# Kernel tuning notes

Hardware: AMD Instinct MI355X
Metric: run time of the kernel (lower is better)

The kernel has to match this reference:

```python
import jax, jax.numpy as jnp
import numpy as np

C = 256

def setup_inputs() -> dict:
    key = jax.random.key(0)
    ks = jax.random.split(key, 9)
    B, H, W = 32, 32, 32
    s = C ** -0.5  # init scale for weights
    inputs = jax.random.normal(ks[0], (B, H, W, C), jnp.float32)
    Wq = jax.random.normal(ks[1], (C, C), jnp.float32) * s
    Wk = jax.random.normal(ks[2], (C, C), jnp.float32) * s
    Wv = jax.random.normal(ks[3], (C, C), jnp.float32) * s
    Wo = jax.random.normal(ks[4], (C, C), jnp.float32) * s
    bq = jnp.zeros((C,), jnp.float32)
    bk = jnp.zeros((C,), jnp.float32)
    bv = jnp.zeros((C,), jnp.float32)
    bo = jnp.zeros((C,), jnp.float32)
    return {"inputs": inputs, "Wq": Wq, "bq": bq, "Wk": Wk, "bk": bk,
            "Wv": Wv, "bv": bv, "Wo": Wo, "bo": bo}

def reference(inputs, Wq, bq, Wk, bk, Wv, bv, Wo, bo):
    B, H, W, c = inputs.shape
    scale = jnp.float32(c) ** -0.5
    x = inputs.reshape(B, H * W, c)           # 1x1 conv == per-pixel matmul
    q = x @ Wq + bq                           # [B, HW, C]
    k = x @ Wk + bk
    v = x @ Wv + bv
    scores = jnp.einsum('bnc,bmc->bnm', q, k) * scale  # [B, HW, HW]
    attn = jax.nn.softmax(scores, axis=-1)
    attended = jnp.einsum('bnm,bmc->bnc', attn, v)     # [B, HW, C]
    out = attended @ Wo + bo
    return out.reshape(B, H, W, c)
```

## Files before the change

kernel.cpp:

```cpp
#include <hip/hip_runtime.h>
#include <hip/hip_bf16.h>

typedef __bf16 bf16;
typedef __bf16 bf16x4 __attribute__((ext_vector_type(4)));
typedef __bf16 bf16x8 __attribute__((ext_vector_type(8)));
typedef float f32x4 __attribute__((ext_vector_type(4)));

#define SM_C 0.09016994374947424f

__global__ __launch_bounds__(256) void transpose_w(
    const float* __restrict__ Wq, const float* __restrict__ Wk,
    const float* __restrict__ Wv, const float* __restrict__ Wo,
    bf16* __restrict__ Wt)
{
    int idx = blockIdx.x * 256 + threadIdx.x;
    int m = idx >> 16, r = idx & 65535;
    int n = r >> 8, k = r & 255;
    const float* W = (m == 0) ? Wq : (m == 1) ? Wk : (m == 2) ? Wv : Wo;
    Wt[(size_t)m * 65536 + n * 256 + k] = (bf16)W[k * 256 + n];
}

__global__ __launch_bounds__(256, 3) void qkv_gemm(
    const float* __restrict__ X, const bf16* __restrict__ Wt,
    const float* __restrict__ bq, const float* __restrict__ bk,
    const float* __restrict__ bv,
    bf16* __restrict__ Qo, bf16* __restrict__ Ko, bf16* __restrict__ Vto)
{
    __shared__ bf16 Xs[128 * 72];
    __shared__ bf16 Ws_[128 * 72];

    const int t    = threadIdx.x;
    const int lane = t & 63, wv = t >> 6;
    const int quad = lane >> 4, l16 = lane & 15;
    const int bm   = blockIdx.x;
    const int bn   = blockIdx.y;
    const int proj = bn >> 1;

    const bf16* W = Wt + (size_t)proj * 65536 + (size_t)(bn & 1) * 32768;
    const float* bias = (proj == 0) ? bq : (proj == 1) ? bk : bv;

    const int m0 = t >> 3;
    const int c0 = (t & 7) * 8;

    const f32x4 zero = {0.0f, 0.0f, 0.0f, 0.0f};
    f32x4 acc[2][8];
#pragma unroll
    for (int i = 0; i < 2; ++i)
#pragma unroll
        for (int j = 0; j < 8; ++j) acc[i][j] = zero;

    f32x4 xa[4], xb[4]; bf16x8 wp[4];
#pragma unroll
    for (int p = 0; p < 4; ++p) {
        const float* px = X + (size_t)(bm * 128 + m0 + p * 32) * 256 + c0;
        xa[p] = *(const f32x4*)px; xb[p] = *(const f32x4*)(px + 4);
        wp[p] = *(const bf16x8*)(W + (size_t)(m0 + p * 32) * 256 + c0);
    }

    for (int kt = 0; kt < 4; ++kt) {
#pragma unroll
        for (int p = 0; p < 4; ++p) {
            bf16x8 r;
#pragma unroll
            for (int j = 0; j < 4; ++j) { r[j] = (bf16)xa[p][j]; r[j + 4] = (bf16)xb[p][j]; }
            *(bf16x8*)(Xs + (m0 + p * 32) * 72 + c0) = r;
            *(bf16x8*)(Ws_ + (m0 + p * 32) * 72 + c0) = wp[p];
        }
        __syncthreads();

        if (kt < 3) {
#pragma unroll
            for (int p = 0; p < 4; ++p) {
                const float* px = X + (size_t)(bm * 128 + m0 + p * 32) * 256 + (kt + 1) * 64 + c0;
                xa[p] = *(const f32x4*)px; xb[p] = *(const f32x4*)(px + 4);
                wp[p] = *(const bf16x8*)(W + (size_t)(m0 + p * 32) * 256 + (kt + 1) * 64 + c0);
            }
        }

#pragma unroll
        for (int ks = 0; ks < 2; ++ks) {
            bf16x8 a[2], bb[8];
#pragma unroll
            for (int mt = 0; mt < 2; ++mt)
                a[mt] = *(const bf16x8*)(Xs + (wv * 32 + mt * 16 + l16) * 72 + ks * 32 + quad * 8);
#pragma unroll
            for (int nt = 0; nt < 8; ++nt)
                bb[nt] = *(const bf16x8*)(Ws_ + (nt * 16 + l16) * 72 + ks * 32 + quad * 8);
#pragma unroll
            for (int mt = 0; mt < 2; ++mt)
#pragma unroll
                for (int nt = 0; nt < 8; ++nt)
                    acc[mt][nt] = __builtin_amdgcn_mfma_f32_16x16x32_bf16(
                        a[mt], bb[nt], acc[mt][nt], 0, 0, 0);
        }
        __syncthreads();
    }

#pragma unroll
    for (int nt = 0; nt < 8; ++nt) {
        int col = (bn & 1) * 128 + nt * 16 + l16;
        float bvv = bias[col];
#pragma unroll
        for (int mt = 0; mt < 2; ++mt) {
            int grow0 = bm * 128 + wv * 32 + mt * 16 + quad * 4;
            if (proj == 2) {
                bf16x4 pk;
#pragma unroll
                for (int r = 0; r < 4; ++r) pk[r] = (bf16)(acc[mt][nt][r] + bvv);
                int b = grow0 >> 10, m = grow0 & 1023;
                *(bf16x4*)(Vto + (size_t)b * 262144 + (size_t)col * 1024 + m) = pk;
            } else {
                bf16* dst = (proj == 0) ? Qo : Ko;
#pragma unroll
                for (int r = 0; r < 4; ++r)
                    dst[(size_t)(grow0 + r) * 256 + col] = (bf16)(acc[mt][nt][r] + bvv);
            }
        }
    }
}

__global__ __launch_bounds__(512, 2) void flash_attn(
    const bf16* __restrict__ Qr, const bf16* __restrict__ K,
    const bf16* __restrict__ Vt, const bf16* __restrict__ Wo,
    const float* __restrict__ bo, float* __restrict__ out)
{
    __shared__ __align__(16) char smem[142336];
    bf16* const Ksp0 = (bf16*)(smem);
    bf16* const Ksp1 = (bf16*)(smem + 16896);
    bf16* const Vsp0 = (bf16*)(smem + 33792);
    bf16* const Vsp1 = (bf16*)(smem + 54272);
    bf16* const Os   = (bf16*)(smem);
    bf16* const Wos  = (bf16*)(smem + 74752);

    const int t    = threadIdx.x;
    const int lane = t & 63, wv = t >> 6;
    const int quad = lane >> 4, l16 = lane & 15;
    const int b  = blockIdx.x;
    const int qt = blockIdx.y;

    char* const Pb = smem + 74752 + wv * 1024;

    bf16x8 qf[8];
    const size_t qrow = (size_t)b * 1024 + qt * 128 + wv * 16 + l16;
#pragma unroll
    for (int ks = 0; ks < 8; ++ks)
        qf[ks] = *(const bf16x8*)(Qr + qrow * 256 + ks * 32 + quad * 8);

    const f32x4 zero = {0.0f, 0.0f, 0.0f, 0.0f};
    f32x4 o[16];
#pragma unroll
    for (int n = 0; n < 16; ++n) o[n] = zero;
    float lst[4] = {0.f, 0.f, 0.f, 0.f};

    const int kv0 = t >> 4, kc0 = (t & 15) * 8;
    const int vc0 = t >> 1, vm0 = (t & 1) * 8;

    bf16x8 kp[2], vp[2];
#pragma unroll
    for (int p = 0; p < 2; ++p) {
        kp[p] = *(const bf16x8*)(K + (size_t)(b * 1024 + kv0) * 256 + kc0 + p * 128);
        vp[p] = *(const bf16x8*)(Vt + (size_t)b * 262144 + (size_t)vc0 * 1024 + vm0 + p * 16);
    }
#pragma unroll
    for (int p = 0; p < 2; ++p) {
        *(bf16x8*)(Ksp0 + kv0 * 264 + kc0 + p * 128) = kp[p];
        *(bf16x8*)(Vsp0 + vc0 * 40 + vm0 + p * 16) = vp[p];
    }
#pragma unroll
    for (int p = 0; p < 2; ++p) {
        kp[p] = *(const bf16x8*)(K + (size_t)(b * 1024 + 32 + kv0) * 256 + kc0 + p * 128);
        vp[p] = *(const bf16x8*)(Vt + (size_t)b * 262144 + (size_t)vc0 * 1024 + 32 + vm0 + p * 16);
    }

    for (int j = 0; j < 32; ++j) {
        const bf16* Kb = (j & 1) ? Ksp1 : Ksp0;
        const bf16* Vb = (j & 1) ? Vsp1 : Vsp0;
        __syncthreads();

        f32x4 s[2];
        s[0] = zero; s[1] = zero;
#pragma unroll
        for (int ks = 0; ks < 8; ++ks) {
#pragma unroll
            for (int n = 0; n < 2; ++n) {
                bf16x8 bfr = *(const bf16x8*)(Kb + (n * 16 + l16) * 264 + ks * 32 + quad * 8);
                s[n] = __builtin_amdgcn_mfma_f32_16x16x32_bf16(qf[ks], bfr, s[n], 0, 0, 0);
            }
        }

        if (j < 31) {
            bf16* Kn = (j & 1) ? Ksp0 : Ksp1;
            bf16* Vn = (j & 1) ? Vsp0 : Vsp1;
#pragma unroll
            for (int p = 0; p < 2; ++p) {
                *(bf16x8*)(Kn + kv0 * 264 + kc0 + p * 128) = kp[p];
                *(bf16x8*)(Vn + vc0 * 40 + vm0 + p * 16) = vp[p];
            }
            if (j < 30) {
#pragma unroll
                for (int p = 0; p < 2; ++p) {
                    kp[p] = *(const bf16x8*)(K + (size_t)(b * 1024 + (j + 2) * 32 + kv0) * 256 + kc0 + p * 128);
                    vp[p] = *(const bf16x8*)(Vt + (size_t)b * 262144 + (size_t)vc0 * 1024 + (j + 2) * 32 + vm0 + p * 16);
                }
            }
        }

#pragma unroll
        for (int n = 0; n < 2; ++n) {
#pragma unroll
            for (int r = 0; r < 4; ++r) {
                float pv = __builtin_amdgcn_exp2f(s[n][r] * SM_C);
                lst[r] += pv;
                int row = quad * 4 + r;
                *(bf16*)(Pb + ((row * 64 + n * 32 + l16 * 2) ^ ((row & 7) << 4))) = (bf16)pv;
            }
        }

        bf16x8 af = *(const bf16x8*)(Pb + ((l16 * 64 + quad * 16) ^ ((l16 & 7) << 4)));
#pragma unroll
        for (int n = 0; n < 16; ++n) {
            bf16x8 bfr = *(const bf16x8*)(Vb + (n * 16 + l16) * 40 + quad * 8);
            o[n] = __builtin_amdgcn_mfma_f32_16x16x32_bf16(af, bfr, o[n], 0, 0, 0);
        }
    }

    __syncthreads();

    float inv[4];
#pragma unroll
    for (int r = 0; r < 4; ++r) {
        float l = lst[r];
#pragma unroll
        for (int off = 1; off < 16; off <<= 1)
            l += __shfl_xor(l, off, 64);
        inv[r] = 1.0f / l;
    }
#pragma unroll
    for (int n = 0; n < 16; ++n)
#pragma unroll
        for (int r = 0; r < 4; ++r)
            Os[(wv * 16 + quad * 4 + r) * 264 + n * 16 + l16] = (bf16)(o[n][r] * inv[r]);

    const int rh = (wv & 1) * 64;
    const int nq = wv >> 1;
    const size_t orow0 = (size_t)b * 1024 + qt * 128 + rh;

#pragma unroll
    for (int h = 0; h < 2; ++h) {
        if (h) __syncthreads();
#pragma unroll
        for (int i = 0; i < 8; ++i) {
            int c = t + i * 512;
            int row = c >> 5, c8 = (c & 31) * 8;
            *(bf16x8*)(Wos + row * 264 + c8) =
                *(const bf16x8*)(Wo + (size_t)(h * 128 + row) * 256 + c8);
        }
        __syncthreads();

        f32x4 acc[4][2];
#pragma unroll
        for (int mt = 0; mt < 4; ++mt) { acc[mt][0] = zero; acc[mt][1] = zero; }

#pragma unroll
        for (int ks = 0; ks < 8; ++ks) {
            bf16x8 a[4], bb[2];
#pragma unroll
            for (int mt = 0; mt < 4; ++mt)
                a[mt] = *(const bf16x8*)(Os + (rh + mt * 16 + l16) * 264 + ks * 32 + quad * 8);
#pragma unroll
            for (int nt = 0; nt < 2; ++nt)
                bb[nt] = *(const bf16x8*)(Wos + (nq * 32 + nt * 16 + l16) * 264 + ks * 32 + quad * 8);
#pragma unroll
            for (int mt = 0; mt < 4; ++mt)
#pragma unroll
                for (int nt = 0; nt < 2; ++nt)
                    acc[mt][nt] = __builtin_amdgcn_mfma_f32_16x16x32_bf16(
                        a[mt], bb[nt], acc[mt][nt], 0, 0, 0);
        }

#pragma unroll
        for (int nt = 0; nt < 2; ++nt) {
            int col = h * 128 + nq * 32 + nt * 16 + l16;
            float bvv = bo[col];
#pragma unroll
            for (int mt = 0; mt < 4; ++mt) {
#pragma unroll
                for (int r = 0; r < 4; ++r) {
                    size_t row = orow0 + mt * 16 + quad * 4 + r;
                    out[row * 256 + col] = acc[mt][nt][r] + bvv;
                }
            }
        }
    }
}

extern "C" void kernel_launch(void* const* d_in, const int* in_sizes, int n_in,
                              void* d_out, int out_size, void* d_ws, size_t ws_size,
                              hipStream_t stream)
{
    (void)in_sizes; (void)n_in; (void)out_size; (void)ws_size;
    const float* X  = (const float*)d_in[0];
    const float* Wq = (const float*)d_in[1];
    const float* bq = (const float*)d_in[2];
    const float* Wk = (const float*)d_in[3];
    const float* bk = (const float*)d_in[4];
    const float* Wv = (const float*)d_in[5];
    const float* bv = (const float*)d_in[6];
    const float* Wo = (const float*)d_in[7];
    const float* bo = (const float*)d_in[8];
    float* out = (float*)d_out;

    const size_t NTOK = (size_t)32768 * 256;

    bf16* Wt  = (bf16*)d_ws;
    bf16* Qw  = (bf16*)d_ws + 262144;
    bf16* Kw  = Qw + NTOK;
    bf16* Vtw = Kw + NTOK;

    transpose_w<<<1024, 256, 0, stream>>>(Wq, Wk, Wv, Wo, Wt);
    qkv_gemm   <<<dim3(256, 6), 256, 0, stream>>>(X, Wt, bq, bk, bv, Qw, Kw, Vtw);
    flash_attn <<<dim3(32, 8),  512, 0, stream>>>(Qw, Kw, Vtw, Wt + 3 * 65536, bo, out);
}
```

Before: 181.8 us.

## Split KV sequence across two wave groups with direct-to-LDS K loads

The attention kernel now splits its 8 waves into two groups that each handle alternating KV tiles, with every wave processing 32 query rows instead of 16. K tiles are loaded with global_load_lds into a swizzled LDS layout, while V stays register-staged. The partial O accumulators and row sums are merged through shared memory before normalization. The weight transpose is also rewritten as a tiled, coalesced shared-memory transpose. This gives more reuse of each K/V fragment across MFMAs, at the cost of more registers, a larger LDS footprint and an extra reduction phase.

```diff
diff --git a/kernel.cpp b/kernel.cpp
--- a/kernel.cpp
+++ b/kernel.cpp
@@ -2,22 +2,39 @@
 #include <hip/hip_bf16.h>
 
 typedef __bf16 bf16;
+typedef __bf16 bf16x2 __attribute__((ext_vector_type(2)));
 typedef __bf16 bf16x4 __attribute__((ext_vector_type(4)));
 typedef __bf16 bf16x8 __attribute__((ext_vector_type(8)));
 typedef float f32x4 __attribute__((ext_vector_type(4)));
 
 #define SM_C 0.09016994374947424f
+
+typedef __attribute__((address_space(1))) const void as1_void;
+typedef __attribute__((address_space(3))) void as3_void;
 
 __global__ __launch_bounds__(256) void transpose_w(
     const float* __restrict__ Wq, const float* __restrict__ Wk,
     const float* __restrict__ Wv, const float* __restrict__ Wo,
     bf16* __restrict__ Wt)
 {
-    int idx = blockIdx.x * 256 + threadIdx.x;
-    int m = idx >> 16, r = idx & 65535;
-    int n = r >> 8, k = r & 255;
+    __shared__ float T[32][33];
+    const int bid = blockIdx.x;
+    const int m = bid >> 6, tile = bid & 63;
+    const int tn0 = (tile >> 3) * 32, tk0 = (tile & 7) * 32;
     const float* W = (m == 0) ? Wq : (m == 1) ? Wk : (m == 2) ? Wv : Wo;
-    Wt[(size_t)m * 65536 + n * 256 + k] = (bf16)W[k * 256 + n];
+
+    const int t = threadIdx.x;
+    const int r = t >> 3, c4 = (t & 7) * 4;
+
+    f32x4 v = *(const f32x4*)(W + (size_t)(tk0 + r) * 256 + tn0 + c4);
+#pragma unroll
+    for (int j = 0; j < 4; ++j) T[r][c4 + j] = v[j];
+    __syncthreads();
+
+    bf16x4 ov;
+#pragma unroll
+    for (int j = 0; j < 4; ++j) ov[j] = (bf16)T[c4 + j][r];
+    *(bf16x4*)(Wt + (size_t)m * 65536 + (size_t)(tn0 + r) * 256 + tk0 + c4) = ov;
 }
 
 __global__ __launch_bounds__(256, 3) void qkv_gemm(
@@ -124,123 +141,190 @@
     const bf16* __restrict__ Vt, const bf16* __restrict__ Wo,
     const float* __restrict__ bo, float* __restrict__ out)
 {
-    __shared__ __align__(16) char smem[142336];
-    bf16* const Ksp0 = (bf16*)(smem);
-    bf16* const Ksp1 = (bf16*)(smem + 16896);
-    bf16* const Vsp0 = (bf16*)(smem + 33792);
-    bf16* const Vsp1 = (bf16*)(smem + 54272);
-    bf16* const Os   = (bf16*)(smem);
-    bf16* const Wos  = (bf16*)(smem + 74752);
+    __shared__ __align__(16) char smem[155648];
 
     const int t    = threadIdx.x;
     const int lane = t & 63, wv = t >> 6;
     const int quad = lane >> 4, l16 = lane & 15;
+    const int g    = wv >> 2, wl = wv & 3;
+    const int gt   = t & 255;
     const int b  = blockIdx.x;
     const int qt = blockIdx.y;
 
-    char* const Pb = smem + 74752 + wv * 1024;
-
-    bf16x8 qf[8];
-    const size_t qrow = (size_t)b * 1024 + qt * 128 + wv * 16 + l16;
-#pragma unroll
-    for (int ks = 0; ks < 8; ++ks)
-        qf[ks] = *(const bf16x8*)(Qr + qrow * 256 + ks * 32 + quad * 8);
+    char* const KsB = smem + g * 73728;
+    char* const VsB = smem + g * 73728 + 32768;
+    char* const Pb  = smem + 147456 + wv * 1024;
+    const int psw = (l16 & 7) << 4;
+
+    bf16x8 qf[2][8];
+#pragma unroll
+    for (int mt = 0; mt < 2; ++mt) {
+        const bf16* qp = Qr + ((size_t)b * 1024 + qt * 128 + wl * 32 + mt * 16 + l16) * 256 + quad * 8;
+#pragma unroll
+        for (int ks = 0; ks < 8; ++ks)
+            qf[mt][ks] = *(const bf16x8*)(qp + ks * 32);
+    }
 
     const f32x4 zero = {0.0f, 0.0f, 0.0f, 0.0f};
-    f32x4 o[16];
-#pragma unroll
-    for (int n = 0; n < 16; ++n) o[n] = zero;
-    float lst[4] = {0.f, 0.f, 0.f, 0.f};
-
-    const int kv0 = t >> 4, kc0 = (t & 15) * 8;
-    const int vc0 = t >> 1, vm0 = (t & 1) * 8;
-
-    bf16x8 kp[2], vp[2];
-#pragma unroll
-    for (int p = 0; p < 2; ++p) {
-        kp[p] = *(const bf16x8*)(K + (size_t)(b * 1024 + kv0) * 256 + kc0 + p * 128);
-        vp[p] = *(const bf16x8*)(Vt + (size_t)b * 262144 + (size_t)vc0 * 1024 + vm0 + p * 16);
-    }
-#pragma unroll
-    for (int p = 0; p < 2; ++p) {
-        *(bf16x8*)(Ksp0 + kv0 * 264 + kc0 + p * 128) = kp[p];
-        *(bf16x8*)(Vsp0 + vc0 * 40 + vm0 + p * 16) = vp[p];
-    }
-#pragma unroll
-    for (int p = 0; p < 2; ++p) {
-        kp[p] = *(const bf16x8*)(K + (size_t)(b * 1024 + 32 + kv0) * 256 + kc0 + p * 128);
-        vp[p] = *(const bf16x8*)(Vt + (size_t)b * 262144 + (size_t)vc0 * 1024 + 32 + vm0 + p * 16);
-    }
-
-    for (int j = 0; j < 32; ++j) {
-        const bf16* Kb = (j & 1) ? Ksp1 : Ksp0;
-        const bf16* Vb = (j & 1) ? Vsp1 : Vsp0;
+    f32x4 o[2][16];
+#pragma unroll
+    for (int mt = 0; mt < 2; ++mt)
+#pragma unroll
+        for (int n = 0; n < 16; ++n) o[mt][n] = zero;
+    float lst[2] = {0.f, 0.f};
+
+    const int vc  = gt >> 1;
+    const int vk8 = (gt & 1) * 8;
+    bf16x8 vp[4];
+
+    auto gloadK = [&](int T, int buf) {
+#pragma unroll
+        for (int p = 0; p < 4; ++p) {
+            int chunk = wl * 4 + p;
+            int row   = chunk * 2 + (lane >> 5);
+            int w16   = (lane & 31) ^ (row & 7);
+            const bf16* gsrc = K + ((size_t)b * 1024 + T * 32 + row) * 256 + w16 * 8;
+            __builtin_amdgcn_global_load_lds((as1_void*)gsrc,
+                (as3_void*)(KsB + buf * 16384 + chunk * 1024), 16, 0, 0);
+        }
+    };
+    auto vload = [&](int T) {
+#pragma unroll
+        for (int p = 0; p < 4; ++p) {
+            int c = vc + 128 * (p >> 1), k8 = vk8 + (p & 1) * 16;
+            vp[p] = *(const bf16x8*)(Vt + (size_t)b * 262144 + (size_t)c * 1024 + T * 32 + k8);
+        }
+    };
+    auto vcommit = [&](int buf) {
+#pragma unroll
+        for (int p = 0; p < 4; ++p) {
+            int c = vc + 128 * (p >> 1), k8 = vk8 + (p & 1) * 16;
+            *(bf16x8*)(VsB + buf * 20480 + c * 80 + k8 * 2) = vp[p];
+        }
+    };
+
+    gloadK(g, 0);
+    vload(g); vcommit(0); vload(g + 2);
+
+    for (int i = 0; i < 16; ++i) {
+        const int buf = i & 1;
         __syncthreads();
 
-        f32x4 s[2];
-        s[0] = zero; s[1] = zero;
+        if (i < 15) {
+            gloadK(g + 2 * (i + 1), buf ^ 1);
+            vcommit(buf ^ 1);
+            if (i < 14) vload(g + 2 * (i + 2));
+        }
+
+        f32x4 s[2][2];
+        s[0][0] = zero; s[0][1] = zero; s[1][0] = zero; s[1][1] = zero;
+        const char* Kbuf = KsB + buf * 16384;
 #pragma unroll
         for (int ks = 0; ks < 8; ++ks) {
 #pragma unroll
             for (int n = 0; n < 2; ++n) {
-                bf16x8 bfr = *(const bf16x8*)(Kb + (n * 16 + l16) * 264 + ks * 32 + quad * 8);
-                s[n] = __builtin_amdgcn_mfma_f32_16x16x32_bf16(qf[ks], bfr, s[n], 0, 0, 0);
-            }
-        }
-
-        if (j < 31) {
-            bf16* Kn = (j & 1) ? Ksp0 : Ksp1;
-            bf16* Vn = (j & 1) ? Vsp0 : Vsp1;
-#pragma unroll
-            for (int p = 0; p < 2; ++p) {
-                *(bf16x8*)(Kn + kv0 * 264 + kc0 + p * 128) = kp[p];
-                *(bf16x8*)(Vn + vc0 * 40 + vm0 + p * 16) = vp[p];
-            }
-            if (j < 30) {
-#pragma unroll
-                for (int p = 0; p < 2; ++p) {
-                    kp[p] = *(const bf16x8*)(K + (size_t)(b * 1024 + (j + 2) * 32 + kv0) * 256 + kc0 + p * 128);
-                    vp[p] = *(const bf16x8*)(Vt + (size_t)b * 262144 + (size_t)vc0 * 1024 + (j + 2) * 32 + vm0 + p * 16);
+                bf16x8 kb = *(const bf16x8*)(Kbuf + (n * 16 + l16) * 512 + ((ks * 64 + quad * 16) ^ psw));
+                s[0][n] = __builtin_amdgcn_mfma_f32_16x16x32_bf16(kb, qf[0][ks], s[0][n], 0, 0, 0);
+                s[1][n] = __builtin_amdgcn_mfma_f32_16x16x32_bf16(kb, qf[1][ks], s[1][n], 0, 0, 0);
+            }
+        }
+
+        bf16x8 af[2];
+#pragma unroll
+        for (int mt = 0; mt < 2; ++mt) {
+#pragma unroll
+            for (int n = 0; n < 2; ++n) {
+#pragma unroll
+                for (int h = 0; h < 2; ++h) {
+                    float p0 = __builtin_amdgcn_exp2f(s[mt][n][2 * h] * SM_C);
+                    float p1 = __builtin_amdgcn_exp2f(s[mt][n][2 * h + 1] * SM_C);
+                    lst[mt] += p0 + p1;
+                    bf16x2 pk; pk[0] = (bf16)p0; pk[1] = (bf16)p1;
+                    *(bf16x2*)(Pb + ((l16 * 64 + n * 32 + quad * 8 + h * 4) ^ psw)) = pk;
                 }
             }
-        }
-
-#pragma unroll
-        for (int n = 0; n < 2; ++n) {
-#pragma unroll
-            for (int r = 0; r < 4; ++r) {
-                float pv = __builtin_amdgcn_exp2f(s[n][r] * SM_C);
-                lst[r] += pv;
-                int row = quad * 4 + r;
-                *(bf16*)(Pb + ((row * 64 + n * 32 + l16 * 2) ^ ((row & 7) << 4))) = (bf16)pv;
-            }
-        }
-
-        bf16x8 af = *(const bf16x8*)(Pb + ((l16 * 64 + quad * 16) ^ ((l16 & 7) << 4)));
+            af[mt] = *(const bf16x8*)(Pb + ((l16 * 64 + quad * 16) ^ psw));
+        }
+
+        const char* Vbuf = VsB + buf * 20480;
 #pragma unroll
         for (int n = 0; n < 16; ++n) {
-            bf16x8 bfr = *(const bf16x8*)(Vb + (n * 16 + l16) * 40 + quad * 8);
-            o[n] = __builtin_amdgcn_mfma_f32_16x16x32_bf16(af, bfr, o[n], 0, 0, 0);
-        }
-    }
-
-    __syncthreads();
-
-    float inv[4];
-#pragma unroll
-    for (int r = 0; r < 4; ++r) {
-        float l = lst[r];
-#pragma unroll
-        for (int off = 1; off < 16; off <<= 1)
-            l += __shfl_xor(l, off, 64);
-        inv[r] = 1.0f / l;
-    }
-#pragma unroll
-    for (int n = 0; n < 16; ++n)
-#pragma unroll
-        for (int r = 0; r < 4; ++r)
-            Os[(wv * 16 + quad * 4 + r) * 264 + n * 16 + l16] = (bf16)(o[n][r] * inv[r]);
-
+            bf16x8 vb = *(const bf16x8*)(Vbuf + (n * 16 + l16) * 80 + quad * 16);
+            o[0][n] = __builtin_amdgcn_mfma_f32_16x16x32_bf16(af[0], vb, o[0][n], 0, 0, 0);
+            o[1][n] = __builtin_amdgcn_mfma_f32_16x16x32_bf16(af[1], vb, o[1][n], 0, 0, 0);
+        }
+    }
+
+    __syncthreads();
+
+#pragma unroll
+    for (int mt = 0; mt < 2; ++mt) {
+        lst[mt] += __shfl_xor(lst[mt], 16, 64);
+        lst[mt] += __shfl_xor(lst[mt], 32, 64);
+    }
+
+    float* const scr  = (float*)(smem + 67584);
+    float* const lstS = (float*)(smem + 135168);
+    bf16*  const Os   = (bf16*)smem;
+
+    if (g == 1) {
+        if (quad == 0) {
+            lstS[wl * 32 + l16]      = lst[0];
+            lstS[wl * 32 + 16 + l16] = lst[1];
+        }
+#pragma unroll
+        for (int mt = 0; mt < 2; ++mt)
+#pragma unroll
+            for (int n = 0; n < 8; ++n)
+                *(f32x4*)(scr + (size_t)(n * 16 + l16) * 132 + wl * 32 + mt * 16 + quad * 4) = o[mt][n];
+    }
+    __syncthreads();
+    if (g == 0) {
+        lst[0] += lstS[wl * 32 + l16];
+        lst[1] += lstS[wl * 32 + 16 + l16];
+#pragma unroll
+        for (int mt = 0; mt < 2; ++mt)
+#pragma unroll
+            for (int n = 0; n < 8; ++n) {
+                f32x4 m = *(const f32x4*)(scr + (size_t)(n * 16 + l16) * 132 + wl * 32 + mt * 16 + quad * 4);
+                o[mt][n] += m;
+            }
+    }
+    __syncthreads();
+    if (g == 1) {
+#pragma unroll
+        for (int mt = 0; mt < 2; ++mt)
+#pragma unroll
+            for (int n = 8; n < 16; ++n)
+                *(f32x4*)(scr + (size_t)((n - 8) * 16 + l16) * 132 + wl * 32 + mt * 16 + quad * 4) = o[mt][n];
+    }
+    __syncthreads();
+    if (g == 0) {
+#pragma unroll
+        for (int mt = 0; mt < 2; ++mt)
+#pragma unroll
+            for (int n = 8; n < 16; ++n) {
+                f32x4 m = *(const f32x4*)(scr + (size_t)((n - 8) * 16 + l16) * 132 + wl * 32 + mt * 16 + quad * 4);
+                o[mt][n] += m;
+            }
+        float inv[2][4];
+#pragma unroll
+        for (int mt = 0; mt < 2; ++mt)
+#pragma unroll
+            for (int r = 0; r < 4; ++r)
+                inv[mt][r] = 1.0f / __shfl(lst[mt], quad * 4 + r, 64);
+#pragma unroll
+        for (int mt = 0; mt < 2; ++mt)
+#pragma unroll
+            for (int n = 0; n < 16; ++n)
+#pragma unroll
+                for (int r = 0; r < 4; ++r)
+                    Os[(size_t)(wl * 32 + mt * 16 + quad * 4 + r) * 264 + n * 16 + l16] =
+                        (bf16)(o[mt][n][r] * inv[mt][r]);
+    }
+    __syncthreads();
+
+    bf16* const Wos = (bf16*)(smem + 67584);
     const int rh = (wv & 1) * 64;
     const int nq = wv >> 1;
     const size_t orow0 = (size_t)b * 1024 + qt * 128 + rh;
@@ -266,7 +350,7 @@
             bf16x8 a[4], bb[2];
 #pragma unroll
             for (int mt = 0; mt < 4; ++mt)
-                a[mt] = *(const bf16x8*)(Os + (rh + mt * 16 + l16) * 264 + ks * 32 + quad * 8);
+                a[mt] = *(const bf16x8*)(Os + (size_t)(rh + mt * 16 + l16) * 264 + ks * 32 + quad * 8);
 #pragma unroll
             for (int nt = 0; nt < 2; ++nt)
                 bb[nt] = *(const bf16x8*)(Wos + (nq * 32 + nt * 16 + l16) * 264 + ks * 32 + quad * 8);
@@ -317,7 +401,7 @@
     bf16* Kw  = Qw + NTOK;
     bf16* Vtw = Kw + NTOK;
 
-    transpose_w<<<1024, 256, 0, stream>>>(Wq, Wk, Wv, Wo, Wt);
+    transpose_w<<<256, 256, 0, stream>>>(Wq, Wk, Wv, Wo, Wt);
     qkv_gemm   <<<dim3(256, 6), 256, 0, stream>>>(X, Wt, bq, bk, bv, Qw, Kw, Vtw);
     flash_attn <<<dim3(32, 8),  512, 0, stream>>>(Qw, Kw, Vtw, Wt + 3 * 65536, bo, out);
 }
```

Measured after the change: 199.7 us. 9.8% more time.
